# Kernel tuning notes

Measured on AMD Instinct MI355X. Metric: run time of the kernel, lower is better.

Reference implementation:

```python
import jax, jax.numpy as jnp
import numpy as np

GS = 128      # quantization group size along K (in_features)
EPS = 1e-8

def setup_inputs() -> dict:
    key = jax.random.key(0)
    k1, k2, k3, k4 = jax.random.split(key, 4)
    B, S, K, N = 4, 2048, 4096, 4096
    x = jax.random.normal(k1, (B, S, K), dtype=jnp.float32)
    weight = jax.random.normal(k2, (N, K), dtype=jnp.float32) * 0.02   # torch Linear layout [out, in]
    bias = jax.random.normal(k3, (N,), dtype=jnp.float32) * 0.01
    # per-group (K//gs) x per-out-channel quant steps, strictly positive
    step_scales = jax.random.uniform(k4, (K // GS, N), dtype=jnp.float32, minval=0.01, maxval=0.05)
    return {"x": x, "weight": weight, "bias": bias, "step_scales": step_scales}

def reference(x, weight, bias, step_scales):
    # w: [K, N] (forward transposes the Linear weight)
    w = weight.T
    K, N = w.shape
    G = K // GS
    wg = w.reshape(G, GS, N)                       # group along K
    s = step_scales[:, None, :] + EPS              # [G, 1, N]
    # group-quantized dequant: round-to-step per (group, out-channel)
    q = jnp.round(wg / s)
    w_dq = (q * s).reshape(K, N)
    out = jnp.einsum('bsk,kn->bsn', x, w_dq)
    if bias is not None:
        out = out + bias
    return out
```

## Files before the change

kernel.cpp:

```cpp
#include <hip/hip_runtime.h>
#include <hip/hip_bf16.h>
#include <stdint.h>

typedef unsigned short u16;
typedef __bf16 bf16x8 __attribute__((ext_vector_type(8)));
typedef float f32x4 __attribute__((ext_vector_type(4)));
typedef unsigned short u16x8 __attribute__((ext_vector_type(8)));

#define QEPS 1e-8f

__device__ __forceinline__ u16 f32_to_bf16_rne(float f) {
    uint32_t u = __float_as_uint(f);
    u += 0x7fffu + ((u >> 16) & 1u);
    return (u16)(u >> 16);
}

__global__ void cvt_x_bf16(const float* __restrict__ x, u16* __restrict__ xb, int n8) {
    int idx = blockIdx.x * blockDim.x + threadIdx.x;
    if (idx >= n8) return;
    const float4* p = (const float4*)(x + (size_t)idx * 8);
    float4 a = p[0], b = p[1];
    u16x8 r;
    r[0] = f32_to_bf16_rne(a.x); r[1] = f32_to_bf16_rne(a.y);
    r[2] = f32_to_bf16_rne(a.z); r[3] = f32_to_bf16_rne(a.w);
    r[4] = f32_to_bf16_rne(b.x); r[5] = f32_to_bf16_rne(b.y);
    r[6] = f32_to_bf16_rne(b.z); r[7] = f32_to_bf16_rne(b.w);
    *(u16x8*)(xb + (size_t)idx * 8) = r;
}

__global__ void dequant_w_bf16(const float* __restrict__ w, const float* __restrict__ ss,
                               u16* __restrict__ wb, int N, int K) {
    int idx = blockIdx.x * blockDim.x + threadIdx.x;
    int pr = K >> 3;
    if (idx >= N * pr) return;
    int n = idx / pr;
    int k8 = (idx - n * pr) << 3;
    float s = ss[(size_t)(k8 >> 7) * N + n] + QEPS;
    const float4* p = (const float4*)(w + (size_t)n * K + k8);
    float4 a = p[0], b = p[1];
    float v[8] = {a.x, a.y, a.z, a.w, b.x, b.y, b.z, b.w};
    u16x8 r;
#pragma unroll
    for (int i = 0; i < 8; ++i) {
        float q = rintf(v[i] / s);
        r[i] = f32_to_bf16_rne(q * s);
    }
    *(u16x8*)(wb + (size_t)n * K + k8) = r;
}

#define BM 256
#define BN 256
#define SLOTB 32768
#define ABYT 16384
#define LDSB 131072

#define ASYNC16(g, l)                                                                      \
    __builtin_amdgcn_global_load_lds((const __attribute__((address_space(1))) void*)(g),   \
                                     (__attribute__((address_space(3))) void*)(l), 16, 0, 0)
#define VMCNT(n) asm volatile("s_waitcnt vmcnt(" #n ")" ::: "memory")
#define BAR()    __builtin_amdgcn_s_barrier()
#define MFMA(a, b, c) __builtin_amdgcn_mfma_f32_16x16x32_bf16((a), (b), (c), 0, 0, 0)

__global__ __launch_bounds__(512, 2) void gemm_bf16_bt_256(
        const u16* __restrict__ A,
        const u16* __restrict__ B,
        const float* __restrict__ bias,
        float* __restrict__ C,
        int M, int N, int K) {
    extern __shared__ char lds[];
    const int tid  = threadIdx.x;
    const int wave = tid >> 6;
    const int lane = tid & 63;

    const int nwg = gridDim.x;
    const int cpx = nwg >> 3;
    const int bid = blockIdx.x;
    const int swz = (bid & 7) * cpx + (bid >> 3);
    const int nbn = N / BN;
    const int bm  = swz / nbn;
    const int bn  = swz - bm * nbn;

    const int wr = wave >> 2;
    const int wc = wave & 3;

    const int srow  = tid >> 2;
    const int kbsrc = ((tid & 3) << 4) ^ (((tid >> 3) & 3) << 4);
    const char* gA0 = (const char*)A + ((size_t)(bm * BM + srow) * K) * 2 + kbsrc;
    const char* gA1 = (const char*)A + ((size_t)(bm * BM + 128 + srow) * K) * 2 + kbsrc;
    const char* gB0 = (const char*)B + ((size_t)(bn * BN + srow) * K) * 2 + kbsrc;
    const char* gB1 = (const char*)B + ((size_t)(bn * BN + 128 + srow) * K) * 2 + kbsrc;

    auto STAGE = [&](int t) {
        const size_t ko = (size_t)t << 6;
        char* d = lds + ((t & 3) * SLOTB) + (wave << 10);
        ASYNC16(gA0 + ko, d);
        ASYNC16(gA1 + ko, d + 8192);
        ASYNC16(gB0 + ko, d + ABYT);
        ASYNC16(gB1 + ko, d + ABYT + 8192);
    };

    const int kx = ((lane >> 4) ^ ((lane >> 1) & 3)) << 4;
    const char* pa = lds + (size_t)(wr * 128 + (lane & 15)) * 64 + kx;
    const char* pb = lds + ABYT + (size_t)(wc * 64 + (lane & 15)) * 64 + kx;

    f32x4 acc[8][4] = {};

#define RDA(m) (*(const bf16x8*)(pa + bo + (m) * 1024))
#define RDB(n) (*(const bf16x8*)(pb + bo + (n) * 1024))
#define MF4(AF, m)                                                            \
    acc[m][0] = MFMA(AF, b0, acc[m][0]);                                      \
    acc[m][1] = MFMA(AF, b1, acc[m][1]);                                      \
    acc[m][2] = MFMA(AF, b2, acc[m][2]);                                      \
    acc[m][3] = MFMA(AF, b3, acc[m][3]);

#define SLAB(t, DO_STAGE, VMSTMT)                                             \
    {                                                                         \
        const int bo = ((t) & 3) * SLOTB;                                     \
        bf16x8 b0 = RDB(0);                                                   \
        bf16x8 a0 = RDA(0), a1 = RDA(1), a2 = RDA(2);                         \
        bf16x8 b1 = RDB(1), b2 = RDB(2), b3 = RDB(3);                         \
        if (DO_STAGE) STAGE((t) + 3);                                         \
        __builtin_amdgcn_s_setprio(1);                                        \
        MF4(a0, 0)  a0 = RDA(3);                                              \
        MF4(a1, 1)  a1 = RDA(4);                                              \
        MF4(a2, 2)  a2 = RDA(5);                                              \
        MF4(a0, 3)  a0 = RDA(6);                                              \
        MF4(a1, 4)  a1 = RDA(7);                                              \
        MF4(a2, 5)                                                            \
        MF4(a0, 6)                                                            \
        MF4(a1, 7)                                                            \
        __builtin_amdgcn_s_setprio(0);                                        \
        VMSTMT;                                                               \
        BAR();                                                                \
    }

    const int NT = K >> 5;

    STAGE(0); STAGE(1); STAGE(2);
    VMCNT(8);
    BAR();

    for (int t = 0; t < NT - 3; ++t)
        SLAB(t, true, VMCNT(8));
    SLAB(NT - 3, false, VMCNT(4));
    SLAB(NT - 2, false, VMCNT(0));
    SLAB(NT - 1, false, (void)0);

    const int r0 = bm * BM + wr * 128 + ((lane >> 4) << 2);
    const int c0 = bn * BN + wc * 64 + (lane & 15);
    float bv[4];
#pragma unroll
    for (int n = 0; n < 4; ++n) bv[n] = bias[c0 + n * 16];
#pragma unroll
    for (int m = 0; m < 8; ++m)
#pragma unroll
        for (int n = 0; n < 4; ++n)
#pragma unroll
            for (int i = 0; i < 4; ++i)
                C[(size_t)(r0 + m * 16 + i) * N + (c0 + n * 16)] = acc[m][n][i] + bv[n];
}

extern "C" void kernel_launch(void* const* d_in, const int* in_sizes, int n_in,
                              void* d_out, int out_size, void* d_ws, size_t ws_size,
                              hipStream_t stream) {
    const float* x    = (const float*)d_in[0];
    const float* w    = (const float*)d_in[1];
    const float* bias = (const float*)d_in[2];
    const float* ss   = (const float*)d_in[3];
    float* out        = (float*)d_out;

    const int N = in_sizes[2];
    const int K = in_sizes[1] / N;
    const int M = in_sizes[0] / K;

    u16* xb = (u16*)d_ws;
    u16* wb = xb + (size_t)M * K;

    int n8x = (M * K) >> 3;
    cvt_x_bf16<<<(n8x + 255) / 256, 256, 0, stream>>>(x, xb, n8x);

    int n8w = (N * K) >> 3;
    dequant_w_bf16<<<(n8w + 255) / 256, 256, 0, stream>>>(w, ss, wb, N, K);

    (void)hipFuncSetAttribute((const void*)gemm_bf16_bt_256,
                              hipFuncAttributeMaxDynamicSharedMemorySize, LDSB);
    dim3 grid((M / BM) * (N / BN));
    gemm_bf16_bt_256<<<grid, 512, LDSB, stream>>>(xb, wb, bias, out, M, N, K);
}
```

Before: 285.3 us.

## Shrink GEMM tile to 256x128 with 3-stage LDS ring and higher occupancy

Result: slower. 321.2 us (+12.6%).

```diff
diff --git a/kernel.cpp b/kernel.cpp
--- a/kernel.cpp
+++ b/kernel.cpp
@@ -49,10 +49,10 @@
 }
 
 #define BM 256
-#define BN 256
-#define SLOTB 32768
+#define BN 128
+#define SLOTB 24576
 #define ABYT 16384
-#define LDSB 131072
+#define LDSB 73728
 
 #define ASYNC16(g, l)                                                                      \
     __builtin_amdgcn_global_load_lds((const __attribute__((address_space(1))) void*)(g),   \
@@ -61,7 +61,7 @@
 #define BAR()    __builtin_amdgcn_s_barrier()
 #define MFMA(a, b, c) __builtin_amdgcn_mfma_f32_16x16x32_bf16((a), (b), (c), 0, 0, 0)
 
-__global__ __launch_bounds__(512, 2) void gemm_bf16_bt_256(
+__global__ __launch_bounds__(512, 4) void gemm_bf16_bt_v6(
         const u16* __restrict__ A,
         const u16* __restrict__ B,
         const float* __restrict__ bias,
@@ -80,55 +80,58 @@
     const int bm  = swz / nbn;
     const int bn  = swz - bm * nbn;
 
-    const int wr = wave >> 2;
-    const int wc = wave & 3;
+    const int wr = wave >> 1;
+    const int wc = wave & 1;
 
     const int srow  = tid >> 2;
     const int kbsrc = ((tid & 3) << 4) ^ (((tid >> 3) & 3) << 4);
     const char* gA0 = (const char*)A + ((size_t)(bm * BM + srow) * K) * 2 + kbsrc;
     const char* gA1 = (const char*)A + ((size_t)(bm * BM + 128 + srow) * K) * 2 + kbsrc;
     const char* gB0 = (const char*)B + ((size_t)(bn * BN + srow) * K) * 2 + kbsrc;
-    const char* gB1 = (const char*)B + ((size_t)(bn * BN + 128 + srow) * K) * 2 + kbsrc;
 
-    auto STAGE = [&](int t) {
+    auto STAGE = [&](int t, int slot) {
         const size_t ko = (size_t)t << 6;
-        char* d = lds + ((t & 3) * SLOTB) + (wave << 10);
+        char* d = lds + slot * SLOTB + (wave << 10);
         ASYNC16(gA0 + ko, d);
         ASYNC16(gA1 + ko, d + 8192);
         ASYNC16(gB0 + ko, d + ABYT);
-        ASYNC16(gB1 + ko, d + ABYT + 8192);
     };
 
     const int kx = ((lane >> 4) ^ ((lane >> 1) & 3)) << 4;
-    const char* pa = lds + (size_t)(wr * 128 + (lane & 15)) * 64 + kx;
+    const char* pa = lds + (size_t)(wr * 64 + (lane & 15)) * 64 + kx;
     const char* pb = lds + ABYT + (size_t)(wc * 64 + (lane & 15)) * 64 + kx;
 
-    f32x4 acc[8][4] = {};
+    f32x4 acc[4][4] = {};
 
-#define RDA(m) (*(const bf16x8*)(pa + bo + (m) * 1024))
-#define RDB(n) (*(const bf16x8*)(pb + bo + (n) * 1024))
-#define MF4(AF, m)                                                            \
-    acc[m][0] = MFMA(AF, b0, acc[m][0]);                                      \
-    acc[m][1] = MFMA(AF, b1, acc[m][1]);                                      \
-    acc[m][2] = MFMA(AF, b2, acc[m][2]);                                      \
-    acc[m][3] = MFMA(AF, b3, acc[m][3]);
-
-#define SLAB(t, DO_STAGE, VMSTMT)                                             \
+#define SLAB(slot, DO_STAGE, t3, slot3, VMSTMT)                               \
     {                                                                         \
-        const int bo = ((t) & 3) * SLOTB;                                     \
-        bf16x8 b0 = RDB(0);                                                   \
-        bf16x8 a0 = RDA(0), a1 = RDA(1), a2 = RDA(2);                         \
-        bf16x8 b1 = RDB(1), b2 = RDB(2), b3 = RDB(3);                         \
-        if (DO_STAGE) STAGE((t) + 3);                                         \
+        const int bo = (slot) * SLOTB;                                        \
+        bf16x8 b0 = *(const bf16x8*)(pb + bo);                                \
+        bf16x8 b1 = *(const bf16x8*)(pb + bo + 1024);                         \
+        bf16x8 a0 = *(const bf16x8*)(pa + bo);                                \
+        bf16x8 a1 = *(const bf16x8*)(pa + bo + 1024);                         \
+        bf16x8 b2 = *(const bf16x8*)(pb + bo + 2048);                         \
+        bf16x8 b3 = *(const bf16x8*)(pb + bo + 3072);                         \
+        if (DO_STAGE) STAGE(t3, slot3);                                       \
         __builtin_amdgcn_s_setprio(1);                                        \
-        MF4(a0, 0)  a0 = RDA(3);                                              \
-        MF4(a1, 1)  a1 = RDA(4);                                              \
-        MF4(a2, 2)  a2 = RDA(5);                                              \
-        MF4(a0, 3)  a0 = RDA(6);                                              \
-        MF4(a1, 4)  a1 = RDA(7);                                              \
-        MF4(a2, 5)                                                            \
-        MF4(a0, 6)                                                            \
-        MF4(a1, 7)                                                            \
+        acc[0][0] = MFMA(a0, b0, acc[0][0]);                                  \
+        acc[0][1] = MFMA(a0, b1, acc[0][1]);                                  \
+        acc[0][2] = MFMA(a0, b2, acc[0][2]);                                  \
+        acc[0][3] = MFMA(a0, b3, acc[0][3]);                                  \
+        bf16x8 a2 = *(const bf16x8*)(pa + bo + 2048);                         \
+        acc[1][0] = MFMA(a1, b0, acc[1][0]);                                  \
+        acc[1][1] = MFMA(a1, b1, acc[1][1]);                                  \
+        acc[1][2] = MFMA(a1, b2, acc[1][2]);                                  \
+        acc[1][3] = MFMA(a1, b3, acc[1][3]);                                  \
+        bf16x8 a3 = *(const bf16x8*)(pa + bo + 3072);                         \
+        acc[2][0] = MFMA(a2, b0, acc[2][0]);                                  \
+        acc[2][1] = MFMA(a2, b1, acc[2][1]);                                  \
+        acc[2][2] = MFMA(a2, b2, acc[2][2]);                                  \
+        acc[2][3] = MFMA(a2, b3, acc[2][3]);                                  \
+        acc[3][0] = MFMA(a3, b0, acc[3][0]);                                  \
+        acc[3][1] = MFMA(a3, b1, acc[3][1]);                                  \
+        acc[3][2] = MFMA(a3, b2, acc[3][2]);                                  \
+        acc[3][3] = MFMA(a3, b3, acc[3][3]);                                  \
         __builtin_amdgcn_s_setprio(0);                                        \
         VMSTMT;                                                               \
         BAR();                                                                \
@@ -136,23 +139,26 @@
 
     const int NT = K >> 5;
 
-    STAGE(0); STAGE(1); STAGE(2);
-    VMCNT(8);
+    STAGE(0, 0); STAGE(1, 1);
+    VMCNT(3);
     BAR();
 
-    for (int t = 0; t < NT - 3; ++t)
-        SLAB(t, true, VMCNT(8));
-    SLAB(NT - 3, false, VMCNT(4));
-    SLAB(NT - 2, false, VMCNT(0));
-    SLAB(NT - 1, false, (void)0);
+    int s0 = 0, s1 = 1, s2 = 2;
+    for (int t = 0; t < NT - 2; ++t) {
+        SLAB(s0, true, t + 2, s2, VMCNT(3));
+        int tmp = s0; s0 = s1; s1 = s2; s2 = tmp;
+    }
+    SLAB(s0, false, 0, 0, VMCNT(0));
+    { int tmp = s0; s0 = s1; s1 = s2; s2 = tmp; }
+    SLAB(s0, false, 0, 0, (void)0);
 
-    const int r0 = bm * BM + wr * 128 + ((lane >> 4) << 2);
+    const int r0 = bm * BM + wr * 64 + ((lane >> 4) << 2);
     const int c0 = bn * BN + wc * 64 + (lane & 15);
     float bv[4];
 #pragma unroll
     for (int n = 0; n < 4; ++n) bv[n] = bias[c0 + n * 16];
 #pragma unroll
-    for (int m = 0; m < 8; ++m)
+    for (int m = 0; m < 4; ++m)
 #pragma unroll
         for (int n = 0; n < 4; ++n)
 #pragma unroll
@@ -182,8 +188,8 @@
     int n8w = (N * K) >> 3;
     dequant_w_bf16<<<(n8w + 255) / 256, 256, 0, stream>>>(w, ss, wb, N, K);
 
-    (void)hipFuncSetAttribute((const void*)gemm_bf16_bt_256,
+    (void)hipFuncSetAttribute((const void*)gemm_bf16_bt_v6,
                               hipFuncAttributeMaxDynamicSharedMemorySize, LDSB);
     dim3 grid((M / BM) * (N / BN));
-    gemm_bf16_bt_256<<<grid, 512, LDSB, stream>>>(xb, wb, bias, out, M, N, K);
+    gemm_bf16_bt_v6<<<grid, 512, LDSB, stream>>>(xb, wb, bias, out, M, N, K);
 }
```

## Prefetch next K-slab LDS fragments into double-buffered registers during MFMAs

Applied to the files above, without the earlier changes.

Result: faster. 275.6 us (-3.4%).

```diff
diff --git a/kernel.cpp b/kernel.cpp
--- a/kernel.cpp
+++ b/kernel.cpp
@@ -104,31 +104,30 @@
     const char* pb = lds + ABYT + (size_t)(wc * 64 + (lane & 15)) * 64 + kx;
 
     f32x4 acc[8][4] = {};
+    bf16x8 bE[4], aE[4], hE[4], bO[4], aO[4], hO[4];
 
-#define RDA(m) (*(const bf16x8*)(pa + bo + (m) * 1024))
-#define RDB(n) (*(const bf16x8*)(pb + bo + (n) * 1024))
-#define MF4(AF, m)                                                            \
-    acc[m][0] = MFMA(AF, b0, acc[m][0]);                                      \
-    acc[m][1] = MFMA(AF, b1, acc[m][1]);                                      \
-    acc[m][2] = MFMA(AF, b2, acc[m][2]);                                      \
-    acc[m][3] = MFMA(AF, b3, acc[m][3]);
-
-#define SLAB(t, DO_STAGE, VMSTMT)                                             \
+#define SLAB(BC, AC, AH, BN_, AN_, t, DO_STAGE, VMSTMT, DO_NEXT)              \
     {                                                                         \
-        const int bo = ((t) & 3) * SLOTB;                                     \
-        bf16x8 b0 = RDB(0);                                                   \
-        bf16x8 a0 = RDA(0), a1 = RDA(1), a2 = RDA(2);                         \
-        bf16x8 b1 = RDB(1), b2 = RDB(2), b3 = RDB(3);                         \
+        const int boc = ((t) & 3) * SLOTB;                                    \
+        const int bon = (((t) + 1) & 3) * SLOTB;                              \
+        _Pragma("unroll") for (int m = 0; m < 4; ++m)                         \
+            AH[m] = *(const bf16x8*)(pa + boc + (m + 4) * 1024);              \
         if (DO_STAGE) STAGE((t) + 3);                                         \
         __builtin_amdgcn_s_setprio(1);                                        \
-        MF4(a0, 0)  a0 = RDA(3);                                              \
-        MF4(a1, 1)  a1 = RDA(4);                                              \
-        MF4(a2, 2)  a2 = RDA(5);                                              \
-        MF4(a0, 3)  a0 = RDA(6);                                              \
-        MF4(a1, 4)  a1 = RDA(7);                                              \
-        MF4(a2, 5)                                                            \
-        MF4(a0, 6)                                                            \
-        MF4(a1, 7)                                                            \
+        _Pragma("unroll") for (int m = 0; m < 4; ++m)                         \
+        _Pragma("unroll") for (int n = 0; n < 4; ++n)                         \
+            acc[m][n] = MFMA(AC[m], BC[n], acc[m][n]);                        \
+        __builtin_amdgcn_s_setprio(0);                                        \
+        if (DO_NEXT) {                                                        \
+            _Pragma("unroll") for (int n = 0; n < 4; ++n)                     \
+                BN_[n] = *(const bf16x8*)(pb + bon + n * 1024);               \
+            _Pragma("unroll") for (int m = 0; m < 4; ++m)                     \
+                AN_[m] = *(const bf16x8*)(pa + bon + m * 1024);               \
+        }                                                                     \
+        __builtin_amdgcn_s_setprio(1);                                        \
+        _Pragma("unroll") for (int m = 0; m < 4; ++m)                         \
+        _Pragma("unroll") for (int n = 0; n < 4; ++n)                         \
+            acc[m + 4][n] = MFMA(AH[m], BC[n], acc[m + 4][n]);                \
         __builtin_amdgcn_s_setprio(0);                                        \
         VMSTMT;                                                               \
         BAR();                                                                \
@@ -137,14 +136,21 @@
     const int NT = K >> 5;
 
     STAGE(0); STAGE(1); STAGE(2);
-    VMCNT(8);
+    VMCNT(4);
     BAR();
+#pragma unroll
+    for (int n = 0; n < 4; ++n) bE[n] = *(const bf16x8*)(pb + n * 1024);
+#pragma unroll
+    for (int m = 0; m < 4; ++m) aE[m] = *(const bf16x8*)(pa + m * 1024);
 
-    for (int t = 0; t < NT - 3; ++t)
-        SLAB(t, true, VMCNT(8));
-    SLAB(NT - 3, false, VMCNT(4));
-    SLAB(NT - 2, false, VMCNT(0));
-    SLAB(NT - 1, false, (void)0);
+    for (int t = 0; t < NT - 4; t += 2) {
+        SLAB(bE, aE, hE, bO, aO, t,     true, VMCNT(4), true)
+        SLAB(bO, aO, hO, bE, aE, t + 1, true, VMCNT(4), true)
+    }
+    SLAB(bE, aE, hE, bO, aO, NT - 4, true,  VMCNT(4), true)
+    SLAB(bO, aO, hO, bE, aE, NT - 3, false, VMCNT(0), true)
+    SLAB(bE, aE, hE, bO, aO, NT - 2, false, (void)0,  true)
+    SLAB(bO, aO, hO, bE, aE, NT - 1, false, (void)0,  false)
 
     const int r0 = bm * BM + wr * 128 + ((lane >> 4) << 2);
     const int c0 = bn * BN + wc * 64 + (lane & 15);
```
